# Kernel tuning notes

Measured on AMD Instinct MI355X. Metric: run time of the kernel, lower is better.

The kernel has to match this reference:

```python
import jax, jax.numpy as jnp
import numpy as np


def _orthogonal(key, n):
    a = jax.random.normal(key, (n, n), dtype=jnp.float32)
    q, r = jnp.linalg.qr(a)
    # sign correction as in torch.nn.init.orthogonal_
    q = q * jnp.sign(jnp.diag(r))
    return q


def setup_inputs() -> dict:
    key = jax.random.key(0)
    k_x, k_b, k_l = jax.random.split(key, 3)
    bs, seq_len, x_dim = 128, 2048, 256
    x_set = jax.random.normal(k_x, (bs, seq_len, x_dim), dtype=jnp.float32)
    B = _orthogonal(k_b, x_dim)
    Lam = _orthogonal(k_l, x_dim)
    return {"x_set": x_set, "B": B, "Lam": Lam}


def reference(x_set, B, Lam):
    # h_t = tanh(B @ x_t + Lambda @ h_{t-1}), h_0-input = 0
    # torch: bmm(B, x[:,T,None]) == x_t @ B.T for row-vector batch layout
    bs, seq_len, x_dim = x_set.shape

    def step(h, x_t):
        h_new = jnp.tanh(x_t @ B.T + h @ Lam.T)  # [bs, x_dim]
        return h_new, h_new

    h0 = jnp.zeros((bs, x_dim), dtype=x_set.dtype)
    _, hs = jax.lax.scan(step, h0, jnp.swapaxes(x_set, 0, 1))  # [T, bs, x_dim]
    return jnp.swapaxes(hs, 0, 1)  # [bs, T, x_dim]
```

## Files before the change

kernel.cpp:

```cpp
#include <hip/hip_runtime.h>

#define TT 2048
#define DD 256

typedef __fp16 half2_t __attribute__((ext_vector_type(2)));
typedef __fp16 half8_t __attribute__((ext_vector_type(8)));
typedef float f32x4_t __attribute__((ext_vector_type(4)));

static __device__ __forceinline__ float fdot2(half2_t a, half2_t b, float c) {
  return __builtin_amdgcn_fdot2(a, b, c, false);
}

static __device__ __forceinline__ float fast_tanh(float y) {
  float e = __builtin_amdgcn_exp2f(y * 2.885390081777927f);
  return 1.0f - 2.0f * __builtin_amdgcn_rcpf(e + 1.0f);
}

static __device__ __forceinline__ float dpp_xor1(float v) {
  return __builtin_bit_cast(float, __builtin_amdgcn_update_dpp(
      0, __builtin_bit_cast(int, v), 0xB1 , 0xF, 0xF, true));
}
static __device__ __forceinline__ float dpp_xor2(float v) {
  return __builtin_bit_cast(float, __builtin_amdgcn_update_dpp(
      0, __builtin_bit_cast(int, v), 0x4E , 0xF, 0xF, true));
}
static __device__ __forceinline__ float dpp_xor7(float v) {
  return __builtin_bit_cast(float, __builtin_amdgcn_update_dpp(
      0, __builtin_bit_cast(int, v), 0x141 , 0xF, 0xF, true));
}
static __device__ __forceinline__ float dpp_xor8(float v) {
  return __builtin_bit_cast(float, __builtin_amdgcn_update_dpp(
      0, __builtin_bit_cast(int, v), 0x128 , 0xF, 0xF, true));
}

#define BST 264
__global__ __launch_bounds__(512, 2) void rnn_u_gemm(
    const float* __restrict__ X, const float* __restrict__ Bm,
    float* __restrict__ U)
{
  extern __shared__ __fp16 bsh[];
  const int tid = threadIdx.x;

  {
    const int r = tid >> 1, kh = (tid & 1) << 7;
    const float* br = Bm + r * DD + kh;
    __fp16* dst = bsh + r * BST + kh;
#pragma unroll
    for (int c = 0; c < 16; ++c) {
      float4 v0 = *(const float4*)(br + c * 8);
      float4 v1 = *(const float4*)(br + c * 8 + 4);
      uint4 w;
      w.x = __builtin_bit_cast(unsigned int, __builtin_amdgcn_cvt_pkrtz(v0.x, v0.y));
      w.y = __builtin_bit_cast(unsigned int, __builtin_amdgcn_cvt_pkrtz(v0.z, v0.w));
      w.z = __builtin_bit_cast(unsigned int, __builtin_amdgcn_cvt_pkrtz(v1.x, v1.y));
      w.w = __builtin_bit_cast(unsigned int, __builtin_amdgcn_cvt_pkrtz(v1.z, v1.w));
      *(uint4*)(dst + c * 8) = w;
    }
  }
  __syncthreads();

  const int wv = tid >> 6;
  const int l = tid & 63;
  const int l16 = l & 15;
  const int lk = l >> 4;
  const size_t tok0 = (size_t)blockIdx.x * 256 + wv * 32;

  f32x4_t acc[2][16];
#pragma unroll
  for (int m = 0; m < 2; ++m)
#pragma unroll
    for (int n = 0; n < 16; ++n)
      acc[m][n] = (f32x4_t){0.f, 0.f, 0.f, 0.f};

  const float* xA0 = X + (tok0 + l16) * DD + lk * 8;
  const float* xA1 = X + (tok0 + 16 + l16) * DD + lk * 8;

#pragma unroll
  for (int ks = 0; ks < 8; ++ks) {
    float4 a00 = *(const float4*)(xA0 + ks * 32);
    float4 a01 = *(const float4*)(xA0 + ks * 32 + 4);
    float4 a10 = *(const float4*)(xA1 + ks * 32);
    float4 a11 = *(const float4*)(xA1 + ks * 32 + 4);
    half2_t p0 = __builtin_amdgcn_cvt_pkrtz(a00.x, a00.y);
    half2_t p1 = __builtin_amdgcn_cvt_pkrtz(a00.z, a00.w);
    half2_t p2 = __builtin_amdgcn_cvt_pkrtz(a01.x, a01.y);
    half2_t p3 = __builtin_amdgcn_cvt_pkrtz(a01.z, a01.w);
    half2_t r0 = __builtin_amdgcn_cvt_pkrtz(a10.x, a10.y);
    half2_t r1 = __builtin_amdgcn_cvt_pkrtz(a10.z, a10.w);
    half2_t r2 = __builtin_amdgcn_cvt_pkrtz(a11.x, a11.y);
    half2_t r3 = __builtin_amdgcn_cvt_pkrtz(a11.z, a11.w);
    half8_t af0 = {p0[0], p0[1], p1[0], p1[1], p2[0], p2[1], p3[0], p3[1]};
    half8_t af1 = {r0[0], r0[1], r1[0], r1[1], r2[0], r2[1], r3[0], r3[1]};
#pragma unroll
    for (int n = 0; n < 16; ++n) {
      half8_t bf = *(const half8_t*)(bsh + (n * 16 + l16) * BST + ks * 32 + lk * 8);
      acc[0][n] = __builtin_amdgcn_mfma_f32_16x16x32_f16(af0, bf, acc[0][n], 0, 0, 0);
      acc[1][n] = __builtin_amdgcn_mfma_f32_16x16x32_f16(af1, bf, acc[1][n], 0, 0, 0);
    }
  }

#pragma unroll
  for (int m = 0; m < 2; ++m) {
    float* ub = U + (tok0 + m * 16 + lk * 4) * DD + l16;
#pragma unroll
    for (int n = 0; n < 16; ++n)
#pragma unroll
      for (int r = 0; r < 4; ++r)
        ub[(size_t)r * DD + n * 16] = acc[m][n][r];
  }
}

__global__ __launch_bounds__(256, 1) void rnn_scan(
    const float* __restrict__ Lm, float* outp )
{
  const int bb = blockIdx.x;
  const int tid = threadIdx.x;
  const int wid = tid >> 6;
  const int lane = tid & 63;
  const int b0 = lane & 1, b1 = (lane >> 1) & 1, b2 = (lane >> 2) & 1;
  const int b3 = (lane >> 3) & 1, b4 = (lane >> 4) & 1, b5 = (lane >> 5) & 1;
  const int s = lane & 15;
  const int G = (wid << 2) | (b5 << 1) | b4;
  const int jbase = G << 4;
  const int rmap = (b0 << 3) ^ (b1 << 2) ^ (b2 ? 14 : 0) ^ b3;
  const int j_out = jbase + rmap;

  __shared__ __align__(16) __fp16 hbuf[2 * DD];

  half2_t lamw[16][8];
#pragma unroll
  for (int i = 0; i < 16; ++i) {
    const float* lp = Lm + (jbase + (i ^ rmap)) * DD + s * 16;
#pragma unroll
    for (int c = 0; c < 4; ++c) {
      float4 v = *(const float4*)(lp + c * 4);
      lamw[i][2 * c]     = __builtin_amdgcn_cvt_pkrtz(v.x, v.y);
      lamw[i][2 * c + 1] = __builtin_amdgcn_cvt_pkrtz(v.z, v.w);
    }
  }

  const char* hrd = (const char*)hbuf + s * 16;
  const int wbyte = ((b0 ^ b2) << 8) + (G << 4) + ((b1 ^ b2) << 3) + (b2 << 2);
  char* hwr = (char*)hbuf + wbyte;

  const size_t obase = (size_t)bb * (TT * DD) + j_out;

  if (tid < 128) ((unsigned int*)hbuf)[tid] = 0u;
  float up0 = outp[obase + 0 * DD];
  float up1 = outp[obase + 1 * DD];
  float up2 = outp[obase + 2 * DD];
  float up3 = outp[obase + 3 * DD];
  __syncthreads();

#define STEP(t, up, p)                                                         \
  {                                                                            \
    uint4 hv0 = *(const uint4*)(hrd + (p) * 512);                              \
    uint4 hv1 = *(const uint4*)(hrd + (p) * 512 + 256);                        \
    unsigned int hd[8] = {hv0.x, hv0.y, hv0.z, hv0.w,                          \
                          hv1.x, hv1.y, hv1.z, hv1.w};                         \
    float acc[16];                                                             \
    _Pragma("unroll")                                                          \
    for (int i = 0; i < 16; ++i) {                                             \
      float a = 0.f;                                                           \
      _Pragma("unroll")                                                        \
      for (int q = 0; q < 8; ++q)                                              \
        a = fdot2(lamw[i][q], __builtin_bit_cast(half2_t, hd[q]), a);          \
      acc[i] = a;                                                              \
    }                                                                          \
        \
    float r0 = acc[0] + dpp_xor1(acc[8]);                                      \
    float r1 = acc[1] + dpp_xor1(acc[9]);                                      \
    float r2 = acc[2] + dpp_xor1(acc[10]);                                     \
    float r3 = acc[3] + dpp_xor1(acc[11]);                                     \
    float r4 = acc[4] + dpp_xor1(acc[12]);                                     \
    float r5 = acc[5] + dpp_xor1(acc[13]);                                     \
    float r6 = acc[6] + dpp_xor1(acc[14]);                                     \
    float r7 = acc[7] + dpp_xor1(acc[15]);                                     \
    float s0 = r0 + dpp_xor2(r4);                                              \
    float s1 = r1 + dpp_xor2(r5);                                              \
    float s2 = r2 + dpp_xor2(r6);                                              \
    float s3 = r3 + dpp_xor2(r7);                                              \
    float t0 = s0 + dpp_xor7(s2);                                              \
    float t1 = s1 + dpp_xor7(s3);                                              \
    float pre = t0 + dpp_xor8(t1) + (up);                                      \
    float hn = fast_tanh(pre);                                                 \
    outp[obase + (size_t)(t) * DD] = hn;                                       \
    float pn = dpp_xor8(hn);                 \
    if (b3 == 0) {                                                             \
      half2_t pk = __builtin_amdgcn_cvt_pkrtz(hn, pn);                         \
      *(unsigned int*)(hwr + ((p) ^ 1) * 512) =                                \
          __builtin_bit_cast(unsigned int, pk);                                \
    }                                                                          \
    { int tn = (t) + 4; tn = tn > TT - 1 ? TT - 1 : tn;                        \
      up = outp[obase + (size_t)tn * DD]; }                                    \
    __builtin_amdgcn_sched_barrier(0);               \
    asm volatile("s_waitcnt lgkmcnt(0)");                                      \
    __builtin_amdgcn_s_barrier();                                              \
    __builtin_amdgcn_sched_barrier(0);           \
  }

  for (int t = 0; t < TT; t += 4) {
    STEP(t + 0, up0, 0)
    STEP(t + 1, up1, 1)
    STEP(t + 2, up2, 0)
    STEP(t + 3, up3, 1)
  }
#undef STEP
}

extern "C" void kernel_launch(void* const* d_in, const int* in_sizes, int n_in,
                              void* d_out, int out_size, void* d_ws, size_t ws_size,
                              hipStream_t stream) {
  const float* X  = (const float*)d_in[0];
  const float* Bm = (const float*)d_in[1];
  const float* Lm = (const float*)d_in[2];
  float* out = (float*)d_out;

  (void)hipFuncSetAttribute((const void*)rnn_u_gemm,
                            hipFuncAttributeMaxDynamicSharedMemorySize,
                            256 * BST * 2);
  hipLaunchKernelGGL(rnn_u_gemm, dim3(1024), dim3(512), 256 * BST * 2, stream,
                     X, Bm, out);
  hipLaunchKernelGGL(rnn_scan, dim3(128), dim3(256), 0, stream, Lm, out);
}
```

Baseline: 954.2 us.

## Process two batch rows per scan block to amortize barriers and latency

Each scan block now handles two independent batch sequences, interleaving their matvec, reduction and tanh inside one time step and sharing a single barrier per step. The grid shrinks from 128 to 64 blocks. The aim is to hide the per-step latency of the serial chain (LDS read, dot products, DPP reductions, barrier) by giving each wave twice the independent work. The cost is that only 64 of the CUs are used, each step carries more instructions, and register pressure rises.

```diff
diff --git a/kernel.cpp b/kernel.cpp
--- a/kernel.cpp
+++ b/kernel.cpp
@@ -125,7 +125,7 @@
   const int rmap = (b0 << 3) ^ (b1 << 2) ^ (b2 ? 14 : 0) ^ b3;
   const int j_out = jbase + rmap;
 
-  __shared__ __align__(16) __fp16 hbuf[2 * DD];
+  __shared__ __align__(16) __fp16 hbuf[2][2 * DD];
 
   half2_t lamw[16][8];
 #pragma unroll
@@ -139,23 +139,29 @@
     }
   }
 
-  const char* hrd = (const char*)hbuf + s * 16;
+  const char* hrdA = (const char*)hbuf[0] + s * 16;
+  const char* hrdB = (const char*)hbuf[1] + s * 16;
   const int wbyte = ((b0 ^ b2) << 8) + (G << 4) + ((b1 ^ b2) << 3) + (b2 << 2);
-  char* hwr = (char*)hbuf + wbyte;
-
-  const size_t obase = (size_t)bb * (TT * DD) + j_out;
-
-  if (tid < 128) ((unsigned int*)hbuf)[tid] = 0u;
-  float up0 = outp[obase + 0 * DD];
-  float up1 = outp[obase + 1 * DD];
-  float up2 = outp[obase + 2 * DD];
-  float up3 = outp[obase + 3 * DD];
+  char* hwrA = (char*)hbuf[0] + wbyte;
+  char* hwrB = (char*)hbuf[1] + wbyte;
+
+  const size_t obaseA = (size_t)(2 * bb)     * (TT * DD) + j_out;
+  const size_t obaseB = (size_t)(2 * bb + 1) * (TT * DD) + j_out;
+
+  if (tid < 128) ((unsigned int*)hbuf[0])[tid] = 0u;
+  else           ((unsigned int*)hbuf[1])[tid - 128] = 0u;
+  float upA0 = outp[obaseA + 0 * DD];
+  float upA1 = outp[obaseA + 1 * DD];
+  float upA2 = outp[obaseA + 2 * DD];
+  float upA3 = outp[obaseA + 3 * DD];
+  float upB0 = outp[obaseB + 0 * DD];
+  float upB1 = outp[obaseB + 1 * DD];
+  float upB2 = outp[obaseB + 2 * DD];
+  float upB3 = outp[obaseB + 3 * DD];
   __syncthreads();
 
-#define STEP(t, up, p)                                                         \
+#define ROWBODY(hv0, hv1, up, hn_out)                                          \
   {                                                                            \
-    uint4 hv0 = *(const uint4*)(hrd + (p) * 512);                              \
-    uint4 hv1 = *(const uint4*)(hrd + (p) * 512 + 256);                        \
     unsigned int hd[8] = {hv0.x, hv0.y, hv0.z, hv0.w,                          \
                           hv1.x, hv1.y, hv1.z, hv1.w};                         \
     float acc[16];                                                             \
@@ -167,7 +173,6 @@
         a = fdot2(lamw[i][q], __builtin_bit_cast(half2_t, hd[q]), a);          \
       acc[i] = a;                                                              \
     }                                                                          \
-        \
     float r0 = acc[0] + dpp_xor1(acc[8]);                                      \
     float r1 = acc[1] + dpp_xor1(acc[9]);                                      \
     float r2 = acc[2] + dpp_xor1(acc[10]);                                     \
@@ -183,16 +188,33 @@
     float t0 = s0 + dpp_xor7(s2);                                              \
     float t1 = s1 + dpp_xor7(s3);                                              \
     float pre = t0 + dpp_xor8(t1) + (up);                                      \
-    float hn = fast_tanh(pre);                                                 \
-    outp[obase + (size_t)(t) * DD] = hn;                                       \
-    float pn = dpp_xor8(hn);                 \
+    hn_out = fast_tanh(pre);                                                   \
+  }
+
+#define STEP(t, upA, upB, p)                                                   \
+  {                                                                            \
+    uint4 hA0 = *(const uint4*)(hrdA + (p) * 512);                             \
+    uint4 hA1 = *(const uint4*)(hrdA + (p) * 512 + 256);                       \
+    uint4 hB0 = *(const uint4*)(hrdB + (p) * 512);                             \
+    uint4 hB1 = *(const uint4*)(hrdB + (p) * 512 + 256);                       \
+    float hnA, hnB;                                                            \
+    ROWBODY(hA0, hA1, upA, hnA)                                                \
+    ROWBODY(hB0, hB1, upB, hnB)                                                \
+    outp[obaseA + (size_t)(t) * DD] = hnA;                                     \
+    outp[obaseB + (size_t)(t) * DD] = hnB;                                     \
+    float pnA = dpp_xor8(hnA);               \
+    float pnB = dpp_xor8(hnB);                                                 \
     if (b3 == 0) {                                                             \
-      half2_t pk = __builtin_amdgcn_cvt_pkrtz(hn, pn);                         \
-      *(unsigned int*)(hwr + ((p) ^ 1) * 512) =                                \
-          __builtin_bit_cast(unsigned int, pk);                                \
+      half2_t pkA = __builtin_amdgcn_cvt_pkrtz(hnA, pnA);                      \
+      half2_t pkB = __builtin_amdgcn_cvt_pkrtz(hnB, pnB);                      \
+      *(unsigned int*)(hwrA + ((p) ^ 1) * 512) =                               \
+          __builtin_bit_cast(unsigned int, pkA);                               \
+      *(unsigned int*)(hwrB + ((p) ^ 1) * 512) =                               \
+          __builtin_bit_cast(unsigned int, pkB);                               \
     }                                                                          \
     { int tn = (t) + 4; tn = tn > TT - 1 ? TT - 1 : tn;                        \
-      up = outp[obase + (size_t)tn * DD]; }                                    \
+      upA = outp[obaseA + (size_t)tn * DD];                                    \
+      upB = outp[obaseB + (size_t)tn * DD]; }                                  \
     __builtin_amdgcn_sched_barrier(0);               \
     asm volatile("s_waitcnt lgkmcnt(0)");                                      \
     __builtin_amdgcn_s_barrier();                                              \
@@ -200,12 +222,13 @@
   }
 
   for (int t = 0; t < TT; t += 4) {
-    STEP(t + 0, up0, 0)
-    STEP(t + 1, up1, 1)
-    STEP(t + 2, up2, 0)
-    STEP(t + 3, up3, 1)
+    STEP(t + 0, upA0, upB0, 0)
+    STEP(t + 1, upA1, upB1, 1)
+    STEP(t + 2, upA2, upB2, 0)
+    STEP(t + 3, upA3, upB3, 1)
   }
 #undef STEP
+#undef ROWBODY
 }
 
 extern "C" void kernel_launch(void* const* d_in, const int* in_sizes, int n_in,
@@ -221,5 +244,5 @@
                             256 * BST * 2);
   hipLaunchKernelGGL(rnn_u_gemm, dim3(1024), dim3(512), 256 * BST * 2, stream,
                      X, Bm, out);
-  hipLaunchKernelGGL(rnn_scan, dim3(128), dim3(256), 0, stream, Lm, out);
-}
+  hipLaunchKernelGGL(rnn_scan, dim3(64), dim3(256), 0, stream, Lm, out);
+}
```

Result: slower. 1.573 ms (+64.9%).
